# Performance work log

Measured on AMD Instinct MI355X. Metric: run time of the kernel, lower is better.

Reference implementation:

```python
import jax, jax.numpy as jnp
import numpy as np
from jax import lax

WIN = 7                      # skimage default win_size
NP_ = WIN * WIN              # pixels per window (2D)
COV_NORM = NP_ / (NP_ - 1)   # sample covariance normalization (use_sample_covariance=True)
K1, K2 = 0.01, 0.03          # skimage defaults


def setup_inputs() -> dict:
    key = jax.random.key(0)
    k1, k2 = jax.random.split(key)
    B, H, W = 64, 512, 512
    predictions = jax.random.uniform(k1, (B, H, W), dtype=jnp.float32)
    labels = jax.random.uniform(k2, (B, H, W), dtype=jnp.float32)
    return {"predictions": predictions, "labels": labels}


def _mean_filter(x):
    # x: [B, 1, H, W] -> valid 7x7 mean filter. Because skimage crops `pad`
    # border pixels before averaging, a VALID convolution reproduces exactly
    # the pixels that survive the crop (reflect padding never enters them).
    kern = jnp.full((1, 1, WIN, WIN), 1.0 / NP_, dtype=x.dtype)
    return lax.conv_general_dilated(x, kern, (1, 1), 'VALID')


def reference(predictions, labels):
    X = predictions[:, None].astype(jnp.float32)  # [B,1,H,W]
    Y = labels[:, None].astype(jnp.float32)

    # per-sample data_range = max(pred,targ) - min(pred,targ)
    dmax = jnp.maximum(X.max(axis=(1, 2, 3)), Y.max(axis=(1, 2, 3)))
    dmin = jnp.minimum(X.min(axis=(1, 2, 3)), Y.min(axis=(1, 2, 3)))
    dr = (dmax - dmin)[:, None, None, None]       # [B,1,1,1]
    C1 = (K1 * dr) ** 2
    C2 = (K2 * dr) ** 2

    ux = _mean_filter(X)
    uy = _mean_filter(Y)
    uxx = _mean_filter(X * X)
    uyy = _mean_filter(Y * Y)
    uxy = _mean_filter(X * Y)

    vx = COV_NORM * (uxx - ux * ux)
    vy = COV_NORM * (uyy - uy * uy)
    vxy = COV_NORM * (uxy - ux * uy)

    S = ((2.0 * ux * uy + C1) * (2.0 * vxy + C2)) / (
        (ux * ux + uy * uy + C1) * (vx + vy + C2))

    mssim = S.mean(axis=(1, 2, 3))  # per-sample SSIM
    return mssim.mean()             # ssim_total / batch_size
```

## Files before the change

### kernel.cpp

```cpp
#include <hip/hip_runtime.h>

#define Hc     512
#define Wc     512
#define OH     506
#define OW     506
#define NPIX   (Hc * Wc)
#define BATCH  64
#define CHUNKS 32

#define BH     16
#define NBAND  32
#define NW     3
#define WPB    4
#define BLK_PER_STRIP (NBAND / WPB)
#define NSTRIP (BATCH * NW)
#define NBLK   (NSTRIP * BLK_PER_STRIP)
#define STRIPS_PER_XCD (NSTRIP / 8)
#define NPART  NBLK

typedef float f32x2 __attribute__((ext_vector_type(2)));
typedef float f32x4 __attribute__((ext_vector_type(4)));

__global__ __launch_bounds__(256) void mm_part_kernel(
    const float* __restrict__ X, const float* __restrict__ Y,
    float* __restrict__ part)
{
    int blk = blockIdx.x;
    int b   = blk >> 5;
    int ch  = blk & 31;
    size_t base = (size_t)b * NPIX + (size_t)ch * (NPIX / CHUNKS);
    const float4* x4 = (const float4*)(X + base);
    const float4* y4 = (const float4*)(Y + base);
    const int n4 = (NPIX / CHUNKS) / 4;

    float mn = 1e38f, mx = -1e38f;
    for (int i = threadIdx.x; i < n4; i += 256) {
        float4 a = x4[i];
        float4 c = y4[i];
        mn = fminf(mn, fminf(fminf(a.x, a.y), fminf(a.z, a.w)));
        mx = fmaxf(mx, fmaxf(fmaxf(a.x, a.y), fmaxf(a.z, a.w)));
        mn = fminf(mn, fminf(fminf(c.x, c.y), fminf(c.z, c.w)));
        mx = fmaxf(mx, fmaxf(fmaxf(c.x, c.y), fmaxf(c.z, c.w)));
    }
    #pragma unroll
    for (int off = 1; off < 64; off <<= 1) {
        mn = fminf(mn, __shfl_xor(mn, off, 64));
        mx = fmaxf(mx, __shfl_xor(mx, off, 64));
    }
    __shared__ float smn[4], smx[4];
    int lane = threadIdx.x & 63, wid = threadIdx.x >> 6;
    if (lane == 0) { smn[wid] = mn; smx[wid] = mx; }
    __syncthreads();
    if (threadIdx.x == 0) {
        mn = fminf(fminf(smn[0], smn[1]), fminf(smn[2], smn[3]));
        mx = fmaxf(fmaxf(smx[0], smx[1]), fmaxf(smx[2], smx[3]));
        part[2 * blk]     = mn;
        part[2 * blk + 1] = mx;
    }
}

__global__ __launch_bounds__(256, 8) void ssim_stream_kernel(
    const float* __restrict__ X, const float* __restrict__ Y,
    const float* __restrict__ mmpart, float* __restrict__ part)
{
    const int lane = threadIdx.x & 63;
    const int wid  = threadIdx.x >> 6;

    const int lin   = blockIdx.x;
    const int xcd   = lin & 7;
    const int slot  = lin >> 3;
    const int strip_local = slot >> 3;
    const int blk   = slot & 7;
    const int strip = xcd * STRIPS_PER_XCD + strip_local;
    const int img   = strip / NW;
    const int chunk = strip - img * NW;
    const int band  = blk * WPB + wid;

    float mn = 1e38f, mx = -1e38f;
    #pragma unroll
    for (int ch = 0; ch < CHUNKS; ++ch) {
        mn = fminf(mn, mmpart[2 * (img * CHUNKS + ch)]);
        mx = fmaxf(mx, mmpart[2 * (img * CHUNKS + ch) + 1]);
    }
    const float dr  = mx - mn;
    const float C1p = 2401.0f * (0.01f * dr) * (0.01f * dr);
    const float C2p = 2401.0f * (0.03f * dr) * (0.03f * dr);
    const f32x2 C1v = {C1p, C1p};
    const f32x2 C2v = {C2p, C2p};
    const f32x2 k49   = {49.0f, 49.0f};
    const f32x2 covn1 = {49.0f / 48.0f, 49.0f / 48.0f};
    const f32x2 covn2 = {2.0f * 49.0f / 48.0f, 2.0f * 49.0f / 48.0f};

    const int cbase  = (chunk == 0) ? 0 : (chunk == 1) ? 248 : 496;
    const int out_lo = (chunk == 0) ? 0 : (chunk == 1) ? 250 : 498;
    const int out_hi = (chunk == 0) ? 249 : (chunk == 1) ? 497 : 505;

    const int col0  = cbase + 4 * lane;
    const int col0c = (col0 < 508) ? col0 : 508;
    f32x2 vm01, vm23;
    {
        float v[4];
        #pragma unroll
        for (int j = 0; j < 4; ++j) {
            int oc = col0 + j;
            v[j] = (oc >= out_lo && oc <= out_hi) ? 1.0f : 0.0f;
        }
        vm01 = (f32x2){v[0], v[1]};
        vm23 = (f32x2){v[2], v[3]};
    }

    const int oy0 = band * BH;
    const int nvalid = (OH - oy0) < BH ? (OH - oy0) : BH;

    const float* px = X + (size_t)img * NPIX + col0c;
    const float* py = Y + (size_t)img * NPIX + col0c;

    f32x2 Vx[2]  = {{0,0},{0,0}}, Vy[2]  = {{0,0},{0,0}};
    f32x2 Vxy[2] = {{0,0},{0,0}}, Vss[2] = {{0,0},{0,0}};

    #define VADD(xa, ya)                                                     \
    {                                                                        \
        f32x2 xl = (xa).lo, xh = (xa).hi, yl = (ya).lo, yh = (ya).hi;        \
        Vx[0] += xl; Vx[1] += xh; Vy[0] += yl; Vy[1] += yh;                  \
        Vxy[0] += xl * yl; Vxy[1] += xh * yh;                                \
        Vss[0] += xl * xl + yl * yl; Vss[1] += xh * xh + yh * yh;            \
    }
    #define VSUB(xa, ya)                                                     \
    {                                                                        \
        f32x2 xl = (xa).lo, xh = (xa).hi, yl = (ya).lo, yh = (ya).hi;        \
        Vx[0] -= xl; Vx[1] -= xh; Vy[0] -= yl; Vy[1] -= yh;                  \
        Vxy[0] -= xl * yl; Vxy[1] -= xh * yh;                                \
        Vss[0] -= xl * xl + yl * yl; Vss[1] -= xh * xh + yh * yh;            \
    }

    #pragma unroll
    for (int k = 0; k < 6; ++k) {
        f32x4 xa = *(const f32x4*)(px + (size_t)(oy0 + k) * Wc);
        f32x4 ya = *(const f32x4*)(py + (size_t)(oy0 + k) * Wc);
        VADD(xa, ya)
    }

    f32x2 acc2 = {0.f, 0.f};

    #define H7(V, W0, W1, W2, W3)                                            \
    {                                                                        \
        float v0 = V[0].x, v1 = V[0].y, v2 = V[1].x, v3 = V[1].y;            \
        float t01 = v0 + v1, u23 = v2 + v3;                                  \
        float P3 = t01 + v2, P4 = t01 + u23;                                 \
        float A3 = __shfl_down(P3, 1, 64);                                   \
        float A4 = __shfl_down(P4, 1, 64);                                   \
        float B1 = __shfl_down(v0, 2, 64);                                   \
        float B2 = __shfl_down(t01, 2, 64);                                  \
        float cc = u23 + A4;                                                 \
        W0 = P4 + A3;                                                        \
        W1 = cc + v1;                                                        \
        W2 = cc + B1;                                                        \
        W3 = (v3 + A4) + B2;                                                 \
    }

    #define SSIM2(wx, wy, wp, ws, vmv)                                       \
    {                                                                        \
        f32x2 t1  = wx * wy;                                                 \
        f32x2 sq  = wx * wx + wy * wy;                                       \
        f32x2 F1  = t1 + t1 + C1v;                                           \
        f32x2 d1  = k49 * wp - t1;                                           \
        f32x2 F2  = covn2 * d1 + C2v;                                        \
        f32x2 F3  = sq + C1v;                                                \
        f32x2 d2  = k49 * ws - sq;                                           \
        f32x2 F4  = covn1 * d2 + C2v;                                        \
        f32x2 den = F3 * F4;                                                 \
        f32x2 num = F1 * F2;                                                 \
        f32x2 rv  = {__builtin_amdgcn_rcpf(den.x),                           \
                     __builtin_amdgcn_rcpf(den.y)};                          \
        acc2 += num * rv * vmv;                                              \
    }

    const float* pxi = px + (size_t)(oy0 + 6) * Wc;
    const float* pyi = py + (size_t)(oy0 + 6) * Wc;
    const float* pxo = px + (size_t)oy0 * Wc;
    const float* pyo = py + (size_t)oy0 * Wc;

    #pragma unroll 4
    for (int tt = 0; tt < nvalid; ++tt) {
        f32x4 xi = *(const f32x4*)pxi; pxi += Wc;
        f32x4 yi = *(const f32x4*)pyi; pyi += Wc;
        VADD(xi, yi)
        float Wx0, Wx1, Wx2, Wx3;  H7(Vx,  Wx0, Wx1, Wx2, Wx3)
        float Wy0, Wy1, Wy2, Wy3;  H7(Vy,  Wy0, Wy1, Wy2, Wy3)
        float Wp0, Wp1, Wp2, Wp3;  H7(Vxy, Wp0, Wp1, Wp2, Wp3)
        float Ws0, Ws1, Ws2, Ws3;  H7(Vss, Ws0, Ws1, Ws2, Ws3)
        f32x2 wx01 = {Wx0, Wx1}, wx23 = {Wx2, Wx3};
        f32x2 wy01 = {Wy0, Wy1}, wy23 = {Wy2, Wy3};
        f32x2 wp01 = {Wp0, Wp1}, wp23 = {Wp2, Wp3};
        f32x2 ws01 = {Ws0, Ws1}, ws23 = {Ws2, Ws3};
        SSIM2(wx01, wy01, wp01, ws01, vm01)
        SSIM2(wx23, wy23, wp23, ws23, vm23)
        f32x4 xo = *(const f32x4*)pxo; pxo += Wc;
        f32x4 yo = *(const f32x4*)pyo; pyo += Wc;
        VSUB(xo, yo)
    }

    #undef SSIM2
    #undef H7
    #undef VADD
    #undef VSUB

    float acc = acc2.x + acc2.y;
    #pragma unroll
    for (int off = 1; off < 64; off <<= 1)
        acc += __shfl_xor(acc, off, 64);
    __shared__ float sacc[4];
    if (lane == 0) sacc[wid] = acc;
    __syncthreads();
    if (threadIdx.x == 0)
        part[lin] = (sacc[0] + sacc[1]) + (sacc[2] + sacc[3]);
}

__global__ __launch_bounds__(1024) void final_reduce_kernel(
    const float* __restrict__ part, float* __restrict__ out)
{
    __shared__ double sd[1024];
    double s = 0.0;
    for (int i = threadIdx.x; i < NPART; i += 1024)
        s += (double)part[i];
    sd[threadIdx.x] = s;
    __syncthreads();
    for (int off = 512; off > 0; off >>= 1) {
        if (threadIdx.x < off) sd[threadIdx.x] += sd[threadIdx.x + off];
        __syncthreads();
    }
    if (threadIdx.x == 0)
        out[0] = (float)(sd[0] / ((double)BATCH * OH * OW));
}

extern "C" void kernel_launch(void* const* d_in, const int* in_sizes, int n_in,
                              void* d_out, int out_size, void* d_ws, size_t ws_size,
                              hipStream_t stream) {
    const float* X = (const float*)d_in[0];
    const float* Y = (const float*)d_in[1];
    float* out = (float*)d_out;
    float* ws  = (float*)d_ws;

    float* mmpart = ws;
    float* part   = ws + 4096;

    mm_part_kernel<<<BATCH * CHUNKS, 256, 0, stream>>>(X, Y, mmpart);
    ssim_stream_kernel<<<NBLK, 64 * WPB, 0, stream>>>(X, Y, mmpart, part);
    final_reduce_kernel<<<1, 1024, 0, stream>>>(part, out);
}
```

Baseline: 75.78 us.

## Keep sliding-window rows in a register ring buffer instead of reloading them

Each wave now processes a taller band of 28 output rows, and 5 blocks cover the 19 bands of a strip. The last 7 input rows are held in a fully unrolled register ring buffer, so the row leaving the 7-row window is subtracted from registers instead of being loaded again from global memory. This halves the global and L2 load traffic per output row and reduces the overlap rows re-read between bands. In exchange it raises register pressure (occupancy hint lowered to 4 blocks per SM), leaves some waves in the last block with no rows, and launches fewer blocks.

Result: no change. 77.17 us (+1.8%).

```diff
diff --git a/kernel.cpp b/kernel.cpp
--- a/kernel.cpp
+++ b/kernel.cpp
@@ -8,11 +8,11 @@
 #define BATCH  64
 #define CHUNKS 32
 
-#define BH     16
-#define NBAND  32
+#define BH     28
+#define NBAND  19
 #define NW     3
 #define WPB    4
-#define BLK_PER_STRIP (NBAND / WPB)
+#define BLK_PER_STRIP 5
 #define NSTRIP (BATCH * NW)
 #define NBLK   (NSTRIP * BLK_PER_STRIP)
 #define STRIPS_PER_XCD (NSTRIP / 8)
@@ -59,7 +59,7 @@
     }
 }
 
-__global__ __launch_bounds__(256, 8) void ssim_stream_kernel(
+__global__ __launch_bounds__(256, 4) void ssim_stream_kernel(
     const float* __restrict__ X, const float* __restrict__ Y,
     const float* __restrict__ mmpart, float* __restrict__ part)
 {
@@ -69,8 +69,8 @@
     const int lin   = blockIdx.x;
     const int xcd   = lin & 7;
     const int slot  = lin >> 3;
-    const int strip_local = slot >> 3;
-    const int blk   = slot & 7;
+    const int strip_local = slot / BLK_PER_STRIP;
+    const int blk   = slot - strip_local * BLK_PER_STRIP;
     const int strip = xcd * STRIPS_PER_XCD + strip_local;
     const int img   = strip / NW;
     const int chunk = strip - img * NW;
@@ -110,35 +110,10 @@
     }
 
     const int oy0 = band * BH;
-    const int nvalid = (OH - oy0) < BH ? (OH - oy0) : BH;
+    const int nvalid = OH - oy0 < BH ? OH - oy0 : BH;
 
     const float* px = X + (size_t)img * NPIX + col0c;
     const float* py = Y + (size_t)img * NPIX + col0c;
-
-    f32x2 Vx[2]  = {{0,0},{0,0}}, Vy[2]  = {{0,0},{0,0}};
-    f32x2 Vxy[2] = {{0,0},{0,0}}, Vss[2] = {{0,0},{0,0}};
-
-    #define VADD(xa, ya)                                                     \
-    {                                                                        \
-        f32x2 xl = (xa).lo, xh = (xa).hi, yl = (ya).lo, yh = (ya).hi;        \
-        Vx[0] += xl; Vx[1] += xh; Vy[0] += yl; Vy[1] += yh;                  \
-        Vxy[0] += xl * yl; Vxy[1] += xh * yh;                                \
-        Vss[0] += xl * xl + yl * yl; Vss[1] += xh * xh + yh * yh;            \
-    }
-    #define VSUB(xa, ya)                                                     \
-    {                                                                        \
-        f32x2 xl = (xa).lo, xh = (xa).hi, yl = (ya).lo, yh = (ya).hi;        \
-        Vx[0] -= xl; Vx[1] -= xh; Vy[0] -= yl; Vy[1] -= yh;                  \
-        Vxy[0] -= xl * yl; Vxy[1] -= xh * yh;                                \
-        Vss[0] -= xl * xl + yl * yl; Vss[1] -= xh * xh + yh * yh;            \
-    }
-
-    #pragma unroll
-    for (int k = 0; k < 6; ++k) {
-        f32x4 xa = *(const f32x4*)(px + (size_t)(oy0 + k) * Wc);
-        f32x4 ya = *(const f32x4*)(py + (size_t)(oy0 + k) * Wc);
-        VADD(xa, ya)
-    }
 
     f32x2 acc2 = {0.f, 0.f};
 
@@ -175,35 +150,65 @@
         acc2 += num * rv * vmv;                                              \
     }
 
-    const float* pxi = px + (size_t)(oy0 + 6) * Wc;
-    const float* pyi = py + (size_t)(oy0 + 6) * Wc;
-    const float* pxo = px + (size_t)oy0 * Wc;
-    const float* pyo = py + (size_t)oy0 * Wc;
-
-    #pragma unroll 4
-    for (int tt = 0; tt < nvalid; ++tt) {
-        f32x4 xi = *(const f32x4*)pxi; pxi += Wc;
-        f32x4 yi = *(const f32x4*)pyi; pyi += Wc;
-        VADD(xi, yi)
-        float Wx0, Wx1, Wx2, Wx3;  H7(Vx,  Wx0, Wx1, Wx2, Wx3)
-        float Wy0, Wy1, Wy2, Wy3;  H7(Vy,  Wy0, Wy1, Wy2, Wy3)
-        float Wp0, Wp1, Wp2, Wp3;  H7(Vxy, Wp0, Wp1, Wp2, Wp3)
-        float Ws0, Ws1, Ws2, Ws3;  H7(Vss, Ws0, Ws1, Ws2, Ws3)
-        f32x2 wx01 = {Wx0, Wx1}, wx23 = {Wx2, Wx3};
-        f32x2 wy01 = {Wy0, Wy1}, wy23 = {Wy2, Wy3};
-        f32x2 wp01 = {Wp0, Wp1}, wp23 = {Wp2, Wp3};
-        f32x2 ws01 = {Ws0, Ws1}, ws23 = {Ws2, Ws3};
-        SSIM2(wx01, wy01, wp01, ws01, vm01)
-        SSIM2(wx23, wy23, wp23, ws23, vm23)
-        f32x4 xo = *(const f32x4*)pxo; pxo += Wc;
-        f32x4 yo = *(const f32x4*)pyo; pyo += Wc;
-        VSUB(xo, yo)
+    if (nvalid > 0) {
+        f32x2 Vx[2]  = {{0,0},{0,0}}, Vy[2]  = {{0,0},{0,0}};
+        f32x2 Vxy[2] = {{0,0},{0,0}}, Vss[2] = {{0,0},{0,0}};
+        f32x2 rgx[7][2], rgy[7][2];
+
+        #pragma unroll
+        for (int j = 0; j < 6; ++j) {
+            f32x4 xa = *(const f32x4*)(px + (size_t)(oy0 + j) * Wc);
+            f32x4 ya = *(const f32x4*)(py + (size_t)(oy0 + j) * Wc);
+            f32x2 xl = xa.lo, xh = xa.hi, yl = ya.lo, yh = ya.hi;
+            Vx[0] += xl; Vx[1] += xh; Vy[0] += yl; Vy[1] += yh;
+            Vxy[0] += xl * yl; Vxy[1] += xh * yh;
+            Vss[0] += xl * xl + yl * yl; Vss[1] += xh * xh + yh * yh;
+            rgx[j][0] = xl; rgx[j][1] = xh;
+            rgy[j][0] = yl; rgy[j][1] = yh;
+        }
+
+        #pragma unroll
+        for (int g = 0; g < 4; ++g) {
+            #pragma unroll
+            for (int k = 0; k < 7; ++k) {
+                const int tt = g * 7 + k;
+                if (tt < nvalid) {
+                    f32x4 xa = *(const f32x4*)(px + (size_t)(oy0 + tt + 6) * Wc);
+                    f32x4 ya = *(const f32x4*)(py + (size_t)(oy0 + tt + 6) * Wc);
+                    f32x2 xl = xa.lo, xh = xa.hi, yl = ya.lo, yh = ya.hi;
+                    Vx[0] += xl; Vx[1] += xh; Vy[0] += yl; Vy[1] += yh;
+                    Vxy[0] += xl * yl; Vxy[1] += xh * yh;
+                    Vss[0] += xl * xl + yl * yl; Vss[1] += xh * xh + yh * yh;
+
+                    float Wx0, Wx1, Wx2, Wx3;  H7(Vx,  Wx0, Wx1, Wx2, Wx3)
+                    float Wy0, Wy1, Wy2, Wy3;  H7(Vy,  Wy0, Wy1, Wy2, Wy3)
+                    float Wp0, Wp1, Wp2, Wp3;  H7(Vxy, Wp0, Wp1, Wp2, Wp3)
+                    float Ws0, Ws1, Ws2, Ws3;  H7(Vss, Ws0, Ws1, Ws2, Ws3)
+                    f32x2 wx01 = {Wx0, Wx1}, wx23 = {Wx2, Wx3};
+                    f32x2 wy01 = {Wy0, Wy1}, wy23 = {Wy2, Wy3};
+                    f32x2 wp01 = {Wp0, Wp1}, wp23 = {Wp2, Wp3};
+                    f32x2 ws01 = {Ws0, Ws1}, ws23 = {Ws2, Ws3};
+                    SSIM2(wx01, wy01, wp01, ws01, vm01)
+                    SSIM2(wx23, wy23, wp23, ws23, vm23)
+
+                    {
+                        f32x2 ox0 = rgx[k][0], ox1 = rgx[k][1];
+                        f32x2 oy_ = rgy[k][0], oy1 = rgy[k][1];
+                        Vx[0] -= ox0; Vx[1] -= ox1;
+                        Vy[0] -= oy_; Vy[1] -= oy1;
+                        Vxy[0] -= ox0 * oy_; Vxy[1] -= ox1 * oy1;
+                        Vss[0] -= ox0 * ox0 + oy_ * oy_;
+                        Vss[1] -= ox1 * ox1 + oy1 * oy1;
+                    }
+                    rgx[(k + 6) % 7][0] = xl; rgx[(k + 6) % 7][1] = xh;
+                    rgy[(k + 6) % 7][0] = yl; rgy[(k + 6) % 7][1] = yh;
+                }
+            }
+        }
     }
 
     #undef SSIM2
     #undef H7
-    #undef VADD
-    #undef VSUB
 
     float acc = acc2.x + acc2.y;
     #pragma unroll
```

## Replace cross-lane shuffles with packed LDS exchange in horizontal box sum

Applied to the files above, without the earlier changes.

The horizontal 7-tap window sum previously used 16 __shfl_down ops per row (4 per statistic). It now writes packed float4 partial sums for all four statistics to per-wave LDS slots and reads the neighbours' values back with 4 vector LDS loads after an explicit lgkmcnt wait, with zeroed padding slots for the lanes at the end of the wave. This cuts cross-lane ops at the cost of 16KB+ of shared memory per block and volatile LDS round-trips that may reduce occupancy. Separately, the min/max pre-pass uses 16 chunks per image instead of 32, with a matching workspace offset.

Result: slower. 122.9 us (+62.1%).

```diff
diff --git a/kernel.cpp b/kernel.cpp
--- a/kernel.cpp
+++ b/kernel.cpp
@@ -6,7 +6,7 @@
 #define OW     506
 #define NPIX   (Hc * Wc)
 #define BATCH  64
-#define CHUNKS 32
+#define CHUNKS 16
 
 #define BH     16
 #define NBAND  32
@@ -26,8 +26,8 @@
     float* __restrict__ part)
 {
     int blk = blockIdx.x;
-    int b   = blk >> 5;
-    int ch  = blk & 31;
+    int b   = blk >> 4;
+    int ch  = blk & 15;
     size_t base = (size_t)b * NPIX + (size_t)ch * (NPIX / CHUNKS);
     const float4* x4 = (const float4*)(X + base);
     const float4* y4 = (const float4*)(Y + base);
@@ -65,6 +65,21 @@
 {
     const int lane = threadIdx.x & 63;
     const int wid  = threadIdx.x >> 6;
+
+    __shared__ float exA3[WPB][66][4];
+    __shared__ float exA4[WPB][66][4];
+    __shared__ float exV0[WPB][66][4];
+    __shared__ float exT0[WPB][66][4];
+
+    if (lane < 2) {
+        #pragma unroll
+        for (int s = 0; s < 4; ++s) {
+            exA3[wid][64 + lane][s] = 0.f;
+            exA4[wid][64 + lane][s] = 0.f;
+            exV0[wid][64 + lane][s] = 0.f;
+            exT0[wid][64 + lane][s] = 0.f;
+        }
+    }
 
     const int lin   = blockIdx.x;
     const int xcd   = lin & 7;
@@ -142,21 +157,10 @@
 
     f32x2 acc2 = {0.f, 0.f};
 
-    #define H7(V, W0, W1, W2, W3)                                            \
-    {                                                                        \
-        float v0 = V[0].x, v1 = V[0].y, v2 = V[1].x, v3 = V[1].y;            \
-        float t01 = v0 + v1, u23 = v2 + v3;                                  \
-        float P3 = t01 + v2, P4 = t01 + u23;                                 \
-        float A3 = __shfl_down(P3, 1, 64);                                   \
-        float A4 = __shfl_down(P4, 1, 64);                                   \
-        float B1 = __shfl_down(v0, 2, 64);                                   \
-        float B2 = __shfl_down(t01, 2, 64);                                  \
-        float cc = u23 + A4;                                                 \
-        W0 = P4 + A3;                                                        \
-        W1 = cc + v1;                                                        \
-        W2 = cc + B1;                                                        \
-        W3 = (v3 + A4) + B2;                                                 \
-    }
+    #define PREP(V, V1o, V3o, T01o, U23o, P3o, P4o)                          \
+        float V1o = V[0].y, V3o = V[1].y;                                    \
+        float T01o = V[0].x + V[0].y, U23o = V[1].x + V[1].y;                \
+        float P3o = T01o + V[1].x, P4o = T01o + U23o;
 
     #define SSIM2(wx, wy, wp, ws, vmv)                                       \
     {                                                                        \
@@ -180,28 +184,58 @@
     const float* pxo = px + (size_t)oy0 * Wc;
     const float* pyo = py + (size_t)oy0 * Wc;
 
+    volatile f32x4* wrA3 = (volatile f32x4*)&exA3[wid][lane][0];
+    volatile f32x4* wrA4 = (volatile f32x4*)&exA4[wid][lane][0];
+    volatile f32x4* wrV0 = (volatile f32x4*)&exV0[wid][lane][0];
+    volatile f32x4* wrT0 = (volatile f32x4*)&exT0[wid][lane][0];
+    volatile const f32x4* rdA3 = (volatile const f32x4*)&exA3[wid][lane + 1][0];
+    volatile const f32x4* rdA4 = (volatile const f32x4*)&exA4[wid][lane + 1][0];
+    volatile const f32x4* rdV0 = (volatile const f32x4*)&exV0[wid][lane + 2][0];
+    volatile const f32x4* rdT0 = (volatile const f32x4*)&exT0[wid][lane + 2][0];
+
     #pragma unroll 4
     for (int tt = 0; tt < nvalid; ++tt) {
         f32x4 xi = *(const f32x4*)pxi; pxi += Wc;
         f32x4 yi = *(const f32x4*)pyi; pyi += Wc;
         VADD(xi, yi)
-        float Wx0, Wx1, Wx2, Wx3;  H7(Vx,  Wx0, Wx1, Wx2, Wx3)
-        float Wy0, Wy1, Wy2, Wy3;  H7(Vy,  Wy0, Wy1, Wy2, Wy3)
-        float Wp0, Wp1, Wp2, Wp3;  H7(Vxy, Wp0, Wp1, Wp2, Wp3)
-        float Ws0, Ws1, Ws2, Ws3;  H7(Vss, Ws0, Ws1, Ws2, Ws3)
-        f32x2 wx01 = {Wx0, Wx1}, wx23 = {Wx2, Wx3};
-        f32x2 wy01 = {Wy0, Wy1}, wy23 = {Wy2, Wy3};
-        f32x2 wp01 = {Wp0, Wp1}, wp23 = {Wp2, Wp3};
-        f32x2 ws01 = {Ws0, Ws1}, ws23 = {Ws2, Ws3};
+
+        PREP(Vx,  vx1, vx3, tx, ux_, p3x, p4x)
+        PREP(Vy,  vy1, vy3, ty, uy_, p3y, p4y)
+        PREP(Vxy, vp1, vp3, tp, up_, p3p, p4p)
+        PREP(Vss, vs1, vs3, ts, us_, p3s, p4s)
+
+        *wrA3 = (f32x4){p3x, p3y, p3p, p3s};
+        *wrA4 = (f32x4){p4x, p4y, p4p, p4s};
+        *wrV0 = (f32x4){Vx[0].x, Vy[0].x, Vxy[0].x, Vss[0].x};
+        *wrT0 = (f32x4){tx, ty, tp, ts};
+        asm volatile("s_waitcnt lgkmcnt(0)" :: );
+
+        f32x4 rA3 = *rdA3;
+        f32x4 rA4 = *rdA4;
+        f32x4 rV0 = *rdV0;
+        f32x4 rT0 = *rdT0;
+
+        float ccx = ux_ + rA4.x, ccy = uy_ + rA4.y;
+        float ccp = up_ + rA4.z, ccs = us_ + rA4.w;
+        f32x2 wx01 = {p4x + rA3.x, ccx + vx1};
+        f32x2 wx23 = {ccx + rV0.x, (vx3 + rA4.x) + rT0.x};
+        f32x2 wy01 = {p4y + rA3.y, ccy + vy1};
+        f32x2 wy23 = {ccy + rV0.y, (vy3 + rA4.y) + rT0.y};
+        f32x2 wp01 = {p4p + rA3.z, ccp + vp1};
+        f32x2 wp23 = {ccp + rV0.z, (vp3 + rA4.z) + rT0.z};
+        f32x2 ws01 = {p4s + rA3.w, ccs + vs1};
+        f32x2 ws23 = {ccs + rV0.w, (vs3 + rA4.w) + rT0.w};
+
         SSIM2(wx01, wy01, wp01, ws01, vm01)
         SSIM2(wx23, wy23, wp23, ws23, vm23)
+
         f32x4 xo = *(const f32x4*)pxo; pxo += Wc;
         f32x4 yo = *(const f32x4*)pyo; pyo += Wc;
         VSUB(xo, yo)
     }
 
     #undef SSIM2
-    #undef H7
+    #undef PREP
     #undef VADD
     #undef VSUB
 
@@ -242,7 +276,7 @@
     float* ws  = (float*)d_ws;
 
     float* mmpart = ws;
-    float* part   = ws + 4096;
+    float* part   = ws + 2048;
 
     mm_part_kernel<<<BATCH * CHUNKS, 256, 0, stream>>>(X, Y, mmpart);
     ssim_stream_kernel<<<NBLK, 64 * WPB, 0, stream>>>(X, Y, mmpart, part);
```
